# Kernel optimization log

Hardware: AMD Instinct MI355X
Metric: run time of the kernel (lower is better)

## Reference

```python
import jax, jax.numpy as jnp
import numpy as np

V, D, S, L, H, NC = 32000, 768, 1024, 4, 12, 16
HS = D // H
B = 8

def _layernorm(x, w, b, eps=1e-5):
    mu = jnp.mean(x, axis=-1, keepdims=True)
    var = jnp.mean(jnp.square(x - mu), axis=-1, keepdims=True)
    return (x - mu) * jax.lax.rsqrt(var + eps) * w + b


def setup_inputs() -> dict:
    key = jax.random.key(0)
    ks = jax.random.split(key, 24)
    s = 0.02
    inp = {
        "x": jax.random.randint(ks[0], (B, S), 0, V, dtype=jnp.int64) if jax.config.jax_enable_x64 else jax.random.randint(ks[0], (B, S), 0, V, dtype=jnp.int32),
        "attention_mask": jnp.ones((B, S), dtype=jnp.int32),
        "tok_emb": jax.random.normal(ks[1], (V, D), jnp.float32) * s,
        "pos_emb": jax.random.normal(ks[2], (S, D), jnp.float32) * s,
        "Wq": jax.random.normal(ks[3], (L, H, D, HS), jnp.float32) * s,
        "Wk": jax.random.normal(ks[4], (L, H, D, HS), jnp.float32) * s,
        "Wv": jax.random.normal(ks[5], (L, H, D, HS), jnp.float32) * s,
        "Wo": jax.random.normal(ks[6], (L, D, D), jnp.float32) * s,
        "bo": jnp.zeros((L, D), jnp.float32),
        "ln1_w": jnp.ones((L, D), jnp.float32),
        "ln1_b": jnp.zeros((L, D), jnp.float32),
        "ln2_w": jnp.ones((L, D), jnp.float32),
        "ln2_b": jnp.zeros((L, D), jnp.float32),
        "W1": jax.random.normal(ks[7], (L, D, 4 * D), jnp.float32) * s,
        "b1": jnp.zeros((L, 4 * D), jnp.float32),
        "W2": jax.random.normal(ks[8], (L, 4 * D, D), jnp.float32) * s,
        "b2": jnp.zeros((L, D), jnp.float32),
        "lnf_w": jnp.ones((D,), jnp.float32),
        "lnf_b": jnp.zeros((D,), jnp.float32),
        "cW1": jax.random.normal(ks[9], (D, 4 * D), jnp.float32) * s,
        "cb1": jnp.zeros((4 * D,), jnp.float32),
        "cW2": jax.random.normal(ks[10], (4 * D, NC), jnp.float32) * s,
        "cb2": jnp.zeros((NC,), jnp.float32),
    }
    return inp


def reference(x, attention_mask, tok_emb, pos_emb, Wq, Wk, Wv, Wo, bo,
              ln1_w, ln1_b, ln2_w, ln2_b, W1, b1, W2, b2,
              lnf_w, lnf_b, cW1, cb1, cW2, cb2):
    b, s = x.shape
    h = tok_emb[x] + pos_emb[jnp.arange(s)][None, :, :]  # [B,S,D]
    key_mask = (attention_mask == 0)[:, None, None, :]   # [B,1,1,S] masks keys
    scale = jnp.asarray(D, h.dtype) ** -0.5              # NOTE: scales by embed_dim, as in source
    for l in range(L):
        xn = _layernorm(h, ln1_w[l], ln1_b[l])
        q = jnp.einsum('bsd,hde->bhse', xn, Wq[l])
        k = jnp.einsum('bsd,hde->bhse', xn, Wk[l])
        v = jnp.einsum('bsd,hde->bhse', xn, Wv[l])
        wei = jnp.einsum('bhqe,bhke->bhqk', q, k) * scale
        wei = jnp.where(key_mask, -jnp.inf, wei)
        att = jax.nn.softmax(wei, axis=-1)               # dropout = identity (eval)
        out = jnp.einsum('bhqk,bhke->bhqe', att, v)      # [B,H,S,HS]
        out = out.transpose(0, 2, 1, 3).reshape(b, s, D)  # concat heads
        h = h + out @ Wo[l] + bo[l]
        xn2 = _layernorm(h, ln2_w[l], ln2_b[l])
        h = h + jax.nn.relu(xn2 @ W1[l] + b1[l]) @ W2[l] + b2[l]
    h = _layernorm(h, lnf_w, lnf_b)
    last = h[:, -1, :]                                   # pool=None -> last position
    logits = jax.nn.relu(last @ cW1 + cb1) @ cW2 + cb2
    return logits
```

## Files before the change

kernel.cpp:

```cpp
#include <hip/hip_runtime.h>
#include <hip/hip_bf16.h>

#define D_MODEL 768
#define SEQ     1024
#define NB      8
#define NHEAD   12
#define HS      64
#define NLAYER  4
#define DFF     3072
#define NCLS    16
#define MROWS   (NB*SEQ)

typedef float f32x4  __attribute__((ext_vector_type(4)));
typedef short bf16x8 __attribute__((ext_vector_type(8)));

__device__ __forceinline__ short f2bf_s(float x) {
    __hip_bfloat16 h = __float2bfloat16(x);
    union { __hip_bfloat16 h; short s; } u; u.h = h; return u.s;
}

__device__ __forceinline__ void gld16(const void* g, void* l) {
    __builtin_amdgcn_global_load_lds((const __attribute__((address_space(1))) void*)g,
                                     (__attribute__((address_space(3))) void*)l, 16, 0, 0);
}

__global__ __launch_bounds__(256) void embed_kernel(
    const int* __restrict__ x, const float* __restrict__ tok,
    const float* __restrict__ pos, float* __restrict__ h)
{
    int row = blockIdx.x;
    int s   = row & (SEQ - 1);
    int t   = threadIdx.x;
    int id  = x[row];
    const float* te = tok + (size_t)id * D_MODEL;
    const float* pe = pos + (size_t)s  * D_MODEL;
    float* hr = h + (size_t)row * D_MODEL;
    for (int d = t; d < D_MODEL; d += 256) hr[d] = te[d] + pe[d];
}

template<int BF16OUT>
__global__ __launch_bounds__(256) void ln_kernel(
    const float* __restrict__ in, const float* __restrict__ w,
    const float* __restrict__ b, void* __restrict__ outv,
    int row_stride, int row_offset)
{
    __shared__ float red[256];
    int r = blockIdx.x;
    const float* xr = in + (size_t)(r * row_stride + row_offset) * D_MODEL;
    int t = threadIdx.x;
    float v0 = xr[t], v1 = xr[t + 256], v2 = xr[t + 512];
    red[t] = v0 + v1 + v2; __syncthreads();
    for (int off = 128; off; off >>= 1) { if (t < off) red[t] += red[t + off]; __syncthreads(); }
    float mu = red[0] * (1.f / D_MODEL);
    __syncthreads();
    float d0 = v0 - mu, d1 = v1 - mu, d2 = v2 - mu;
    red[t] = d0*d0 + d1*d1 + d2*d2; __syncthreads();
    for (int off = 128; off; off >>= 1) { if (t < off) red[t] += red[t + off]; __syncthreads(); }
    float rstd = rsqrtf(red[0] * (1.f / D_MODEL) + 1e-5f);
    float y0 = d0 * rstd * w[t]       + b[t];
    float y1 = d1 * rstd * w[t + 256] + b[t + 256];
    float y2 = d2 * rstd * w[t + 512] + b[t + 512];
    if (BF16OUT) {
        __hip_bfloat16* yr = (__hip_bfloat16*)outv + (size_t)r * D_MODEL;
        yr[t] = __float2bfloat16(y0); yr[t+256] = __float2bfloat16(y1); yr[t+512] = __float2bfloat16(y2);
    } else {
        float* yr = (float*)outv + (size_t)r * D_MODEL;
        yr[t] = y0; yr[t+256] = y1; yr[t+512] = y2;
    }
}

template<int MODE>
__global__ __launch_bounds__(256) void convw_kernel(
    const float* __restrict__ W, __hip_bfloat16* __restrict__ BT,
    int K, int N, size_t in_stride, size_t out_stride)
{
    __shared__ __hip_bfloat16 sT[64][72];
    W  += (size_t)blockIdx.z * in_stride;
    BT += (size_t)blockIdx.z * out_stride;
    int k0 = blockIdx.x * 64, n0 = blockIdx.y * 64;
    int t = threadIdx.x;
    int kl = t >> 4, nl4 = (t & 15) * 4;
    #pragma unroll
    for (int i = 0; i < 4; i++) {
        int k = k0 + kl + i * 16;
        int n = n0 + nl4;
        const float* src = (MODE == 0) ? (W + (size_t)k * N + n)
                                       : (W + ((size_t)(n >> 6) * K + k) * 64 + (n & 63));
        float4 v = *(const float4*)src;
        sT[nl4 + 0][kl + i*16] = __float2bfloat16(v.x);
        sT[nl4 + 1][kl + i*16] = __float2bfloat16(v.y);
        sT[nl4 + 2][kl + i*16] = __float2bfloat16(v.z);
        sT[nl4 + 3][kl + i*16] = __float2bfloat16(v.w);
    }
    __syncthreads();
    int nl = t >> 2, seg = (t & 3) * 16;
    uint4* dst = (uint4*)(BT + (size_t)(n0 + nl) * K + k0 + seg);
    dst[0] = *(uint4*)&sT[nl][seg];
    dst[1] = *(uint4*)&sT[nl][seg + 8];
}

template<int OMODE>
__global__ __launch_bounds__(256, 3) void gemm128(
    const __hip_bfloat16* __restrict__ A, const __hip_bfloat16* __restrict__ BT,
    const float* __restrict__ bias, const float* __restrict__ res,
    void* __restrict__ Cv, int M, int N, int K, int relu)
{
    __shared__ short sA[128 * 32];
    __shared__ short sB[128 * 32];
    int t = threadIdx.x;
    int wave = t >> 6, lane = t & 63;
    int l16 = lane & 15, quad = (lane >> 4) & 3;
    int wm = wave >> 1, wn = wave & 1;
    int bm = blockIdx.x * 128, bn = blockIdx.y * 128;

    int u = lane >> 2;
    int skey = ((u & 3) ^ ((u >> 2) & 3));
    int sseg = (lane & 3) ^ skey;
    int c0 = wave * 2, c1 = wave * 2 + 1;
    int rA0 = c0 * 16 + u, rA1 = c1 * 16 + u;
    int fkey = ((l16 & 3) ^ ((l16 >> 2) & 3));

    const f32x4 zf = {0.f, 0.f, 0.f, 0.f};
    f32x4 acc[4][4];
    #pragma unroll
    for (int mi = 0; mi < 4; mi++)
        #pragma unroll
        for (int ni = 0; ni < 4; ni++) acc[mi][ni] = zf;

    for (int k0 = 0; k0 < K; k0 += 32) {
        gld16(A  + (size_t)(bm + rA0) * K + k0 + sseg * 8, &sA[c0 * 512]);
        gld16(A  + (size_t)(bm + rA1) * K + k0 + sseg * 8, &sA[c1 * 512]);
        gld16(BT + (size_t)(bn + rA0) * K + k0 + sseg * 8, &sB[c0 * 512]);
        gld16(BT + (size_t)(bn + rA1) * K + k0 + sseg * 8, &sB[c1 * 512]);
        __syncthreads();
        bf16x8 aF[4], bF[4];
        #pragma unroll
        for (int mi = 0; mi < 4; mi++)
            aF[mi] = *(bf16x8*)&sA[(wm * 64 + mi * 16 + l16) * 32 + ((quad ^ fkey) * 8)];
        #pragma unroll
        for (int ni = 0; ni < 4; ni++)
            bF[ni] = *(bf16x8*)&sB[(wn * 64 + ni * 16 + l16) * 32 + ((quad ^ fkey) * 8)];
        #pragma unroll
        for (int ni = 0; ni < 4; ni++)
            #pragma unroll
            for (int mi = 0; mi < 4; mi++)
                acc[mi][ni] = __builtin_amdgcn_mfma_f32_16x16x32_bf16(aF[mi], bF[ni], acc[mi][ni], 0, 0, 0);
        __syncthreads();
    }
    #pragma unroll
    for (int mi = 0; mi < 4; mi++) {
        #pragma unroll
        for (int ni = 0; ni < 4; ni++) {
            int row0 = bm + wm * 64 + mi * 16 + quad * 4;
            int col  = bn + wn * 64 + ni * 16 + l16;
            #pragma unroll
            for (int r = 0; r < 4; r++) {
                int row = row0 + r;
                float v = acc[mi][ni][r];
                if (OMODE != 1 && bias) v += bias[col];
                if (relu) v = fmaxf(v, 0.f);
                if (OMODE == 0) {
                    float* C = (float*)Cv;
                    if (res) v += res[(size_t)row * N + col];
                    C[(size_t)row * N + col] = v;
                } else if (OMODE == 1) {
                    int which = col / D_MODEL, cc = col % D_MODEL;
                    int bb = row >> 10, ss = row & 1023, hh = cc >> 6, e = cc & 63;
                    ((__hip_bfloat16*)Cv)[(size_t)which * MROWS * D_MODEL +
                        (((size_t)(bb * NHEAD + hh)) * SEQ + ss) * HS + e] = __float2bfloat16(v);
                } else {
                    ((__hip_bfloat16*)Cv)[(size_t)row * N + col] = __float2bfloat16(v);
                }
            }
        }
    }
    (void)M;
}

__global__ __launch_bounds__(256) void vtrans_kernel(
    const __hip_bfloat16* __restrict__ vb, __hip_bfloat16* __restrict__ vt)
{
    __shared__ short tile[64][66];
    int bh = blockIdx.x, st = blockIdx.y;
    const short* src = (const short*)vb + ((size_t)bh * SEQ + st * 64) * HS;
    int t = threadIdx.x;
    #pragma unroll
    for (int i = 0; i < 2; i++) {
        int slot = t + i * 256;
        int row = slot >> 3, seg = slot & 7;
        *(uint4*)&tile[row][seg * 8] = *(const uint4*)(src + row * HS + seg * 8);
    }
    __syncthreads();
    short* dst = (short*)vt + (size_t)bh * HS * SEQ + st * 64;
    #pragma unroll
    for (int i = 0; i < 2; i++) {
        int slot = t + i * 256;
        int e = slot >> 3, seg = slot & 7;
        union { uint4 u; short s[8]; } pk;
        #pragma unroll
        for (int j = 0; j < 8; j++) pk.s[j] = tile[seg * 8 + j][e];
        *(uint4*)(dst + (size_t)e * SEQ + seg * 8) = pk.u;
    }
}

__global__ __launch_bounds__(128, 2) void attn_mfma_kernel(
    const __hip_bfloat16* __restrict__ q, const __hip_bfloat16* __restrict__ k,
    const __hip_bfloat16* __restrict__ v, const int* __restrict__ mask,
    __hip_bfloat16* __restrict__ ao)
{
    __shared__ short sK[64 * 64];
    __shared__ short sVT[64 * 64];
    __shared__ short sP[2][64 * 64];
    __shared__ float mskf[SEQ];
    int blk = blockIdx.x;
    int qt8 = blk & 7, bh = blk >> 3;
    int b = bh / NHEAD, hh = bh % NHEAD;
    int t = threadIdx.x, w = t >> 6, lane = t & 63;
    int l16 = lane & 15, quad = lane >> 4;
    const float scale = 0.036084391824351615f;
    const f32x4 zf = {0.f, 0.f, 0.f, 0.f};

    #pragma unroll
    for (int i = 0; i < 8; i++) {
        int idx = t + i * 128;
        mskf[idx] = mask[b * SEQ + idx] ? 0.f : -1e30f;
    }

    int qb0 = qt8 * 128 + w * 64;
    const __hip_bfloat16* qbase = q + ((size_t)bh * SEQ + qb0) * HS;
    bf16x8 qf[4][2];
    #pragma unroll
    for (int qt = 0; qt < 4; qt++)
        #pragma unroll
        for (int s = 0; s < 2; s++)
            qf[qt][s] = *(const bf16x8*)(qbase + (qt * 16 + l16) * HS + s * 32 + quad * 8);

    f32x4 accO[4][4];
    float m_st[4], l_st[4];
    #pragma unroll
    for (int dt = 0; dt < 4; dt++)
        #pragma unroll
        for (int qt = 0; qt < 4; qt++) accO[dt][qt] = zf;
    #pragma unroll
    for (int qt = 0; qt < 4; qt++) { m_st[qt] = -1e30f; l_st[qt] = 0.f; }

    int rowL = lane >> 3;
    int sgl = ((lane & 7) ^ ((lane >> 3) & 7)) * 8;
    const __hip_bfloat16* kg0 = k + ((size_t)bh * SEQ) * HS;
    const __hip_bfloat16* vtg0 = v + (size_t)bh * HS * SEQ;
    short* myP = &sP[w][0];

    for (int kc = 0; kc < 16; kc++) {
        const __hip_bfloat16* kg = kg0 + (size_t)kc * 64 * HS;
        const __hip_bfloat16* vtg = vtg0 + kc * 64;
        #pragma unroll
        for (int i = 0; i < 4; i++) {
            int c = w * 4 + i;
            int rr = c * 8 + rowL;
            gld16(kg + (size_t)rr * HS + sgl, (char*)sK + c * 1024);
            gld16(vtg + (size_t)rr * SEQ + sgl, (char*)sVT + c * 1024);
        }
        __syncthreads();

        bf16x8 vf[4][2];
        #pragma unroll
        for (int dt = 0; dt < 4; dt++)
            #pragma unroll
            for (int s = 0; s < 2; s++)
                vf[dt][s] = *(bf16x8*)&sVT[(dt * 16 + l16) * 64 + (((s * 4 + quad) ^ (l16 & 7)) * 8)];
        f32x4 sc[4][4];
        #pragma unroll
        for (int kt = 0; kt < 4; kt++) {
            bf16x8 kf0 = *(bf16x8*)&sK[(kt * 16 + l16) * 64 + ((quad ^ (l16 & 7)) * 8)];
            bf16x8 kf1 = *(bf16x8*)&sK[(kt * 16 + l16) * 64 + (((4 + quad) ^ (l16 & 7)) * 8)];
            #pragma unroll
            for (int qt = 0; qt < 4; qt++) {
                f32x4 c = __builtin_amdgcn_mfma_f32_16x16x32_bf16(kf0, qf[qt][0], zf, 0, 0, 0);
                sc[kt][qt] = __builtin_amdgcn_mfma_f32_16x16x32_bf16(kf1, qf[qt][1], c, 0, 0, 0);
            }
        }
        #pragma unroll
        for (int kt = 0; kt < 4; kt++) {
            f32x4 mk = *(f32x4*)&mskf[kc * 64 + kt * 16 + quad * 4];
            #pragma unroll
            for (int qt = 0; qt < 4; qt++)
                #pragma unroll
                for (int r = 0; r < 4; r++)
                    sc[kt][qt][r] = sc[kt][qt][r] * scale + mk[r];
        }
        #pragma unroll
        for (int qt = 0; qt < 4; qt++) {
            float rm = -1e30f;
            #pragma unroll
            for (int kt = 0; kt < 4; kt++)
                #pragma unroll
                for (int r = 0; r < 4; r++) rm = fmaxf(rm, sc[kt][qt][r]);
            rm = fmaxf(rm, __shfl_xor(rm, 16));
            rm = fmaxf(rm, __shfl_xor(rm, 32));
            float mnew = fmaxf(m_st[qt], rm);
            float corr = __expf(m_st[qt] - mnew);
            m_st[qt] = mnew;
            float ps = 0.f;
            #pragma unroll
            for (int kt = 0; kt < 4; kt++) {
                union { uint2 u; short s[4]; } pk;
                #pragma unroll
                for (int r = 0; r < 4; r++) {
                    float p = __expf(sc[kt][qt][r] - mnew);
                    ps += p;
                    pk.s[r] = f2bf_s(p);
                }
                *(uint2*)&myP[(qt * 16 + l16) * 64 +
                              (((kt * 2 + (quad >> 1)) ^ (l16 & 7)) * 8) + (quad & 1) * 4] = pk.u;
            }
            ps += __shfl_xor(ps, 16);
            ps += __shfl_xor(ps, 32);
            l_st[qt] = l_st[qt] * corr + ps;
            #pragma unroll
            for (int dt = 0; dt < 4; dt++) accO[dt][qt] *= corr;
        }
        asm volatile("" ::: "memory");
        #pragma unroll
        for (int qt = 0; qt < 4; qt++) {
            bf16x8 pf0 = *(bf16x8*)&myP[(qt * 16 + l16) * 64 + ((quad ^ (l16 & 7)) * 8)];
            bf16x8 pf1 = *(bf16x8*)&myP[(qt * 16 + l16) * 64 + (((4 + quad) ^ (l16 & 7)) * 8)];
            #pragma unroll
            for (int dt = 0; dt < 4; dt++) {
                accO[dt][qt] = __builtin_amdgcn_mfma_f32_16x16x32_bf16(vf[dt][0], pf0, accO[dt][qt], 0, 0, 0);
                accO[dt][qt] = __builtin_amdgcn_mfma_f32_16x16x32_bf16(vf[dt][1], pf1, accO[dt][qt], 0, 0, 0);
            }
        }
        __syncthreads();
    }

    #pragma unroll
    for (int qt = 0; qt < 4; qt++) {
        float inv = 1.f / l_st[qt];
        int row = qb0 + qt * 16 + l16;
        __hip_bfloat16* orow = ao + ((size_t)(b * SEQ + row)) * D_MODEL + hh * HS;
        #pragma unroll
        for (int dt = 0; dt < 4; dt++) {
            union { uint2 u; short s[4]; } pk;
            #pragma unroll
            for (int r = 0; r < 4; r++) pk.s[r] = f2bf_s(accO[dt][qt][r] * inv);
            *(uint2*)(orow + dt * 16 + quad * 4) = pk.u;
        }
    }
}

__global__ __launch_bounds__(256) void fc1_kernel(
    const float* __restrict__ A, const float* __restrict__ W,
    const float* __restrict__ bias, float* __restrict__ out)
{
    __shared__ float sa[D_MODEL];
    int row = blockIdx.x, t = threadIdx.x;
    for (int i = t; i < D_MODEL; i += 256) sa[i] = A[(size_t)row * D_MODEL + i];
    __syncthreads();
    int col = blockIdx.y * 256 + t;
    float s = 0.f;
    #pragma unroll 8
    for (int kk = 0; kk < D_MODEL; kk++) s = fmaf(sa[kk], W[(size_t)kk * DFF + col], s);
    s += bias[col];
    out[(size_t)row * DFF + col] = fmaxf(s, 0.f);
}

__global__ __launch_bounds__(256) void fc2_kernel(
    const float* __restrict__ A, const float* __restrict__ W,
    const float* __restrict__ bias, float* __restrict__ out)
{
    __shared__ float wred[4][NCLS];
    int row = blockIdx.x, t = threadIdx.x;
    int wave = t >> 6, lane = t & 63;
    const float* a = A + (size_t)row * DFF;
    float acc[NCLS];
    #pragma unroll
    for (int c = 0; c < NCLS; c++) acc[c] = 0.f;
    for (int kk = t; kk < DFF; kk += 256) {
        float av = a[kk];
        const float4* wr = (const float4*)(W + (size_t)kk * NCLS);
        float4 w0 = wr[0], w1 = wr[1], w2 = wr[2], w3 = wr[3];
        acc[0]  = fmaf(av, w0.x, acc[0]);  acc[1]  = fmaf(av, w0.y, acc[1]);
        acc[2]  = fmaf(av, w0.z, acc[2]);  acc[3]  = fmaf(av, w0.w, acc[3]);
        acc[4]  = fmaf(av, w1.x, acc[4]);  acc[5]  = fmaf(av, w1.y, acc[5]);
        acc[6]  = fmaf(av, w1.z, acc[6]);  acc[7]  = fmaf(av, w1.w, acc[7]);
        acc[8]  = fmaf(av, w2.x, acc[8]);  acc[9]  = fmaf(av, w2.y, acc[9]);
        acc[10] = fmaf(av, w2.z, acc[10]); acc[11] = fmaf(av, w2.w, acc[11]);
        acc[12] = fmaf(av, w3.x, acc[12]); acc[13] = fmaf(av, w3.y, acc[13]);
        acc[14] = fmaf(av, w3.z, acc[14]); acc[15] = fmaf(av, w3.w, acc[15]);
    }
    #pragma unroll
    for (int c = 0; c < NCLS; c++)
        #pragma unroll
        for (int off = 32; off; off >>= 1) acc[c] += __shfl_down(acc[c], off);
    if (lane == 0)
        #pragma unroll
        for (int c = 0; c < NCLS; c++) wred[wave][c] = acc[c];
    __syncthreads();
    if (t < NCLS)
        out[row * NCLS + t] = wred[0][t] + wred[1][t] + wred[2][t] + wred[3][t] + bias[t];
}

extern "C" void kernel_launch(void* const* d_in, const int* in_sizes, int n_in,
                              void* d_out, int out_size, void* d_ws, size_t ws_size,
                              hipStream_t stream)
{
    const int*   x     = (const int*)  d_in[0];
    const int*   amask = (const int*)  d_in[1];
    const float* tok   = (const float*)d_in[2];
    const float* pos   = (const float*)d_in[3];
    const float* Wq    = (const float*)d_in[4];
    const float* Wk    = (const float*)d_in[5];
    const float* Wv    = (const float*)d_in[6];
    const float* Wo    = (const float*)d_in[7];
    const float* bo    = (const float*)d_in[8];
    const float* ln1w  = (const float*)d_in[9];
    const float* ln1b  = (const float*)d_in[10];
    const float* ln2w  = (const float*)d_in[11];
    const float* ln2b  = (const float*)d_in[12];
    const float* W1    = (const float*)d_in[13];
    const float* b1    = (const float*)d_in[14];
    const float* W2    = (const float*)d_in[15];
    const float* b2    = (const float*)d_in[16];
    const float* lnfw  = (const float*)d_in[17];
    const float* lnfb  = (const float*)d_in[18];
    const float* cW1   = (const float*)d_in[19];
    const float* cb1   = (const float*)d_in[20];
    const float* cW2   = (const float*)d_in[21];
    const float* cb2   = (const float*)d_in[22];

    char* base = (char*)d_ws;
    const size_t MD = (size_t)MROWS * D_MODEL;
    float* h = (float*)base;                         base += MD * 4;
    __hip_bfloat16* xn = (__hip_bfloat16*)base;      base += MD * 2;
    __hip_bfloat16* qb = (__hip_bfloat16*)base;      base += MD * 2;
    __hip_bfloat16* kb = (__hip_bfloat16*)base;      base += MD * 2;
    __hip_bfloat16* vb = (__hip_bfloat16*)base;      base += MD * 2;
    __hip_bfloat16* vT = (__hip_bfloat16*)base;      base += MD * 2;
    __hip_bfloat16* ff = (__hip_bfloat16*)base;      base += (size_t)MROWS * DFF * 2;
    float* lnf = (float*)base;                       base += (size_t)NB * D_MODEL * 4;
    float* cls = (float*)base;                       base += (size_t)NB * DFF * 4;
    __hip_bfloat16* wQKV = (__hip_bfloat16*)base;    base += (size_t)NLAYER * 3 * D_MODEL * D_MODEL * 2;
    __hip_bfloat16* wTo = (__hip_bfloat16*)base;     base += (size_t)NLAYER * D_MODEL * D_MODEL * 2;
    __hip_bfloat16* wT1 = (__hip_bfloat16*)base;     base += (size_t)NLAYER * D_MODEL * DFF * 2;
    __hip_bfloat16* wT2 = (__hip_bfloat16*)base;     base += (size_t)NLAYER * DFF * D_MODEL * 2;

    const size_t SQW = (size_t)D_MODEL * D_MODEL;
    const size_t SFF = (size_t)D_MODEL * DFF;

    convw_kernel<1><<<dim3(12,12,4), 256, 0, stream>>>(Wq, wQKV + 0 * SQW, D_MODEL, D_MODEL, SQW, 3 * SQW);
    convw_kernel<1><<<dim3(12,12,4), 256, 0, stream>>>(Wk, wQKV + 1 * SQW, D_MODEL, D_MODEL, SQW, 3 * SQW);
    convw_kernel<1><<<dim3(12,12,4), 256, 0, stream>>>(Wv, wQKV + 2 * SQW, D_MODEL, D_MODEL, SQW, 3 * SQW);
    convw_kernel<0><<<dim3(12,12,4), 256, 0, stream>>>(Wo, wTo, D_MODEL, D_MODEL, SQW, SQW);
    convw_kernel<0><<<dim3(12,48,4), 256, 0, stream>>>(W1, wT1, D_MODEL, DFF, SFF, SFF);
    convw_kernel<0><<<dim3(48,12,4), 256, 0, stream>>>(W2, wT2, DFF, D_MODEL, SFF, SFF);

    embed_kernel<<<MROWS, 256, 0, stream>>>(x, tok, pos, h);

    dim3 gQKV(MROWS / 128, (3 * D_MODEL) / 128);
    dim3 gD(MROWS / 128, D_MODEL / 128);
    dim3 gF(MROWS / 128, DFF / 128);
    for (int l = 0; l < NLAYER; l++) {
        ln_kernel<1><<<MROWS, 256, 0, stream>>>(h, ln1w + l * D_MODEL, ln1b + l * D_MODEL, xn, 1, 0);
        gemm128<1><<<gQKV, 256, 0, stream>>>(xn, wQKV + l * 3 * SQW, nullptr, nullptr, qb, MROWS, 3 * D_MODEL, D_MODEL, 0);
        vtrans_kernel<<<dim3(NB * NHEAD, SEQ / 64), 256, 0, stream>>>(vb, vT);
        attn_mfma_kernel<<<NB * NHEAD * 8, 128, 0, stream>>>(qb, kb, vT, amask, xn);
        gemm128<0><<<gD, 256, 0, stream>>>(xn, wTo + l * SQW, bo + l * D_MODEL, h, h, MROWS, D_MODEL, D_MODEL, 0);
        ln_kernel<1><<<MROWS, 256, 0, stream>>>(h, ln2w + l * D_MODEL, ln2b + l * D_MODEL, xn, 1, 0);
        gemm128<2><<<gF, 256, 0, stream>>>(xn, wT1 + l * SFF, b1 + l * DFF, nullptr, ff, MROWS, DFF, D_MODEL, 1);
        gemm128<0><<<gD, 256, 0, stream>>>(ff, wT2 + l * SFF, b2 + l * D_MODEL, h, h, MROWS, D_MODEL, DFF, 0);
    }
    ln_kernel<0><<<NB, 256, 0, stream>>>(h, lnfw, lnfb, lnf, SEQ, SEQ - 1);
    fc1_kernel<<<dim3(NB, DFF / 256), 256, 0, stream>>>(lnf, cW1, cb1, cls);
    fc2_kernel<<<NB, 256, 0, stream>>>(cls, cW2, cb2, (float*)d_out);
}
```

Baseline: 1.828 ms.

## Double-buffer GEMM and attention LDS loads, split-K N=768 GEMMs with atomics

Adds double-buffered LDS staging to the generic GEMM and to the attention kernel, so the next K tile's global-to-LDS loads are issued before the MFMAs on the current tile. The two N=768 GEMMs (output projection and FFN down) are split along K into two z-slices that atomically add into the residual stream h. This raises the block count from 384 to 768 so more CUs stay busy. The attention block index is also remapped so each XCD works on the same batch-heads. The changes double the shared memory per block, which may lower occupancy, and the atomics make the float sums order-dependent.

Result: faster. 1.753 ms (-4.1%).

```diff
diff --git a/kernel.cpp b/kernel.cpp
--- a/kernel.cpp
+++ b/kernel.cpp
@@ -105,13 +105,16 @@
     const float* __restrict__ bias, const float* __restrict__ res,
     void* __restrict__ Cv, int M, int N, int K, int relu)
 {
-    __shared__ short sA[128 * 32];
-    __shared__ short sB[128 * 32];
+    __shared__ short sA[2][128 * 32];
+    __shared__ short sB[2][128 * 32];
     int t = threadIdx.x;
     int wave = t >> 6, lane = t & 63;
     int l16 = lane & 15, quad = (lane >> 4) & 3;
     int wm = wave >> 1, wn = wave & 1;
     int bm = blockIdx.x * 128, bn = blockIdx.y * 128;
+
+    int kbeg = 0, kend = K;
+    if (OMODE == 3) { int KS = K >> 1; kbeg = blockIdx.z * KS; kend = kbeg + KS; }
 
     int u = lane >> 2;
     int skey = ((u & 3) ^ ((u >> 2) & 3));
@@ -127,26 +130,36 @@
         #pragma unroll
         for (int ni = 0; ni < 4; ni++) acc[mi][ni] = zf;
 
-    for (int k0 = 0; k0 < K; k0 += 32) {
-        gld16(A  + (size_t)(bm + rA0) * K + k0 + sseg * 8, &sA[c0 * 512]);
-        gld16(A  + (size_t)(bm + rA1) * K + k0 + sseg * 8, &sA[c1 * 512]);
-        gld16(BT + (size_t)(bn + rA0) * K + k0 + sseg * 8, &sB[c0 * 512]);
-        gld16(BT + (size_t)(bn + rA1) * K + k0 + sseg * 8, &sB[c1 * 512]);
-        __syncthreads();
+    #define STAGE(bufi, kk) do { \
+        gld16(A  + (size_t)(bm + rA0) * K + (kk) + sseg * 8, &sA[bufi][c0 * 512]); \
+        gld16(A  + (size_t)(bm + rA1) * K + (kk) + sseg * 8, &sA[bufi][c1 * 512]); \
+        gld16(BT + (size_t)(bn + rA0) * K + (kk) + sseg * 8, &sB[bufi][c0 * 512]); \
+        gld16(BT + (size_t)(bn + rA1) * K + (kk) + sseg * 8, &sB[bufi][c1 * 512]); \
+    } while (0)
+
+    STAGE(0, kbeg);
+    __syncthreads();
+    int buf = 0;
+    for (int k0 = kbeg; k0 < kend; k0 += 32) {
+        int kn = k0 + 32;
+        if (kn < kend) STAGE(buf ^ 1, kn);
         bf16x8 aF[4], bF[4];
         #pragma unroll
         for (int mi = 0; mi < 4; mi++)
-            aF[mi] = *(bf16x8*)&sA[(wm * 64 + mi * 16 + l16) * 32 + ((quad ^ fkey) * 8)];
+            aF[mi] = *(bf16x8*)&sA[buf][(wm * 64 + mi * 16 + l16) * 32 + ((quad ^ fkey) * 8)];
         #pragma unroll
         for (int ni = 0; ni < 4; ni++)
-            bF[ni] = *(bf16x8*)&sB[(wn * 64 + ni * 16 + l16) * 32 + ((quad ^ fkey) * 8)];
+            bF[ni] = *(bf16x8*)&sB[buf][(wn * 64 + ni * 16 + l16) * 32 + ((quad ^ fkey) * 8)];
         #pragma unroll
         for (int ni = 0; ni < 4; ni++)
             #pragma unroll
             for (int mi = 0; mi < 4; mi++)
                 acc[mi][ni] = __builtin_amdgcn_mfma_f32_16x16x32_bf16(aF[mi], bF[ni], acc[mi][ni], 0, 0, 0);
         __syncthreads();
-    }
+        buf ^= 1;
+    }
+    #undef STAGE
+
     #pragma unroll
     for (int mi = 0; mi < 4; mi++) {
         #pragma unroll
@@ -157,6 +170,12 @@
             for (int r = 0; r < 4; r++) {
                 int row = row0 + r;
                 float v = acc[mi][ni][r];
+                if (OMODE == 3) {
+                    float* C = (float*)Cv;
+                    if (blockIdx.z == 0 && bias) v += bias[col];
+                    unsafeAtomicAdd(&C[(size_t)row * N + col], v);
+                    continue;
+                }
                 if (OMODE != 1 && bias) v += bias[col];
                 if (relu) v = fmaxf(v, 0.f);
                 if (OMODE == 0) {
@@ -208,12 +227,14 @@
     const __hip_bfloat16* __restrict__ v, const int* __restrict__ mask,
     __hip_bfloat16* __restrict__ ao)
 {
-    __shared__ short sK[64 * 64];
-    __shared__ short sVT[64 * 64];
+    __shared__ short sK[2][64 * 64];
+    __shared__ short sVT[2][64 * 64];
     __shared__ short sP[2][64 * 64];
     __shared__ float mskf[SEQ];
-    int blk = blockIdx.x;
-    int qt8 = blk & 7, bh = blk >> 3;
+    int bid = blockIdx.x;
+    int xcd = bid & 7, j = bid >> 3;
+    int bh  = ((j >> 3) << 3) | xcd;
+    int qt8 = j & 7;
     int b = bh / NHEAD, hh = bh % NHEAD;
     int t = threadIdx.x, w = t >> 6, lane = t & 63;
     int l16 = lane & 15, quad = lane >> 4;
@@ -250,29 +271,42 @@
     const __hip_bfloat16* vtg0 = v + (size_t)bh * HS * SEQ;
     short* myP = &sP[w][0];
 
+    #pragma unroll
+    for (int i = 0; i < 4; i++) {
+        int c = w * 4 + i;
+        int rr = c * 8 + rowL;
+        gld16(kg0  + (size_t)rr * HS  + sgl, (char*)&sK[0][0]  + c * 1024);
+        gld16(vtg0 + (size_t)rr * SEQ + sgl, (char*)&sVT[0][0] + c * 1024);
+    }
+    __syncthreads();
+
+    int buf = 0;
     for (int kc = 0; kc < 16; kc++) {
-        const __hip_bfloat16* kg = kg0 + (size_t)kc * 64 * HS;
-        const __hip_bfloat16* vtg = vtg0 + kc * 64;
-        #pragma unroll
-        for (int i = 0; i < 4; i++) {
-            int c = w * 4 + i;
-            int rr = c * 8 + rowL;
-            gld16(kg + (size_t)rr * HS + sgl, (char*)sK + c * 1024);
-            gld16(vtg + (size_t)rr * SEQ + sgl, (char*)sVT + c * 1024);
-        }
-        __syncthreads();
+        if (kc < 15) {
+            const __hip_bfloat16* kg  = kg0  + (size_t)(kc + 1) * 64 * HS;
+            const __hip_bfloat16* vtg = vtg0 + (kc + 1) * 64;
+            #pragma unroll
+            for (int i = 0; i < 4; i++) {
+                int c = w * 4 + i;
+                int rr = c * 8 + rowL;
+                gld16(kg  + (size_t)rr * HS  + sgl, (char*)&sK[buf ^ 1][0]  + c * 1024);
+                gld16(vtg + (size_t)rr * SEQ + sgl, (char*)&sVT[buf ^ 1][0] + c * 1024);
+            }
+        }
+        short* cK  = &sK[buf][0];
+        short* cVT = &sVT[buf][0];
 
         bf16x8 vf[4][2];
         #pragma unroll
         for (int dt = 0; dt < 4; dt++)
             #pragma unroll
             for (int s = 0; s < 2; s++)
-                vf[dt][s] = *(bf16x8*)&sVT[(dt * 16 + l16) * 64 + (((s * 4 + quad) ^ (l16 & 7)) * 8)];
+                vf[dt][s] = *(bf16x8*)&cVT[(dt * 16 + l16) * 64 + (((s * 4 + quad) ^ (l16 & 7)) * 8)];
         f32x4 sc[4][4];
         #pragma unroll
         for (int kt = 0; kt < 4; kt++) {
-            bf16x8 kf0 = *(bf16x8*)&sK[(kt * 16 + l16) * 64 + ((quad ^ (l16 & 7)) * 8)];
-            bf16x8 kf1 = *(bf16x8*)&sK[(kt * 16 + l16) * 64 + (((4 + quad) ^ (l16 & 7)) * 8)];
+            bf16x8 kf0 = *(bf16x8*)&cK[(kt * 16 + l16) * 64 + ((quad ^ (l16 & 7)) * 8)];
+            bf16x8 kf1 = *(bf16x8*)&cK[(kt * 16 + l16) * 64 + (((4 + quad) ^ (l16 & 7)) * 8)];
             #pragma unroll
             for (int qt = 0; qt < 4; qt++) {
                 f32x4 c = __builtin_amdgcn_mfma_f32_16x16x32_bf16(kf0, qf[qt][0], zf, 0, 0, 0);
@@ -331,6 +365,7 @@
             }
         }
         __syncthreads();
+        buf ^= 1;
     }
 
     #pragma unroll
@@ -457,17 +492,17 @@
     embed_kernel<<<MROWS, 256, 0, stream>>>(x, tok, pos, h);
 
     dim3 gQKV(MROWS / 128, (3 * D_MODEL) / 128);
-    dim3 gD(MROWS / 128, D_MODEL / 128);
+    dim3 gDS(MROWS / 128, D_MODEL / 128, 2);
     dim3 gF(MROWS / 128, DFF / 128);
     for (int l = 0; l < NLAYER; l++) {
         ln_kernel<1><<<MROWS, 256, 0, stream>>>(h, ln1w + l * D_MODEL, ln1b + l * D_MODEL, xn, 1, 0);
         gemm128<1><<<gQKV, 256, 0, stream>>>(xn, wQKV + l * 3 * SQW, nullptr, nullptr, qb, MROWS, 3 * D_MODEL, D_MODEL, 0);
         vtrans_kernel<<<dim3(NB * NHEAD, SEQ / 64), 256, 0, stream>>>(vb, vT);
         attn_mfma_kernel<<<NB * NHEAD * 8, 128, 0, stream>>>(qb, kb, vT, amask, xn);
-        gemm128<0><<<gD, 256, 0, stream>>>(xn, wTo + l * SQW, bo + l * D_MODEL, h, h, MROWS, D_MODEL, D_MODEL, 0);
+        gemm128<3><<<gDS, 256, 0, stream>>>(xn, wTo + l * SQW, bo + l * D_MODEL, nullptr, h, MROWS, D_MODEL, D_MODEL, 0);
         ln_kernel<1><<<MROWS, 256, 0, stream>>>(h, ln2w + l * D_MODEL, ln2b + l * D_MODEL, xn, 1, 0);
         gemm128<2><<<gF, 256, 0, stream>>>(xn, wT1 + l * SFF, b1 + l * DFF, nullptr, ff, MROWS, DFF, D_MODEL, 1);
-        gemm128<0><<<gD, 256, 0, stream>>>(ff, wT2 + l * SFF, b2 + l * D_MODEL, h, h, MROWS, D_MODEL, DFF, 0);
+        gemm128<3><<<gDS, 256, 0, stream>>>(ff, wT2 + l * SFF, b2 + l * D_MODEL, nullptr, h, MROWS, D_MODEL, DFF, 0);
     }
     ln_kernel<0><<<NB, 256, 0, stream>>>(h, lnfw, lnfb, lnf, SEQ, SEQ - 1);
     fc1_kernel<<<dim3(NB, DFF / 256), 256, 0, stream>>>(lnf, cW1, cb1, cls);
```
